# Kernel optimization log

Hardware: AMD Instinct MI355X
Metric: run time of the kernel (lower is better)

## Reference

```python
import jax, jax.numpy as jnp
import numpy as np
from jax import lax

N = 4667      # num vertices (hardcoded in Spatial_Attention_layer)
B = 4         # batch
T = 8         # raw timesteps; (T-2)*3 == 18 after TimeBlock + concat
C_IN = 2      # input features
TP = 18       # concatenated timesteps
HID = 16      # TimeBlock out channels / PCN fc width
N_ROOTS = 500
BRANCH = 2
DEPTH = 3


def _build_tree():
    # Static stand-in for the P/roots/s2rDic dict-based trajectory tree.
    rng = np.random.RandomState(42)
    roots = rng.choice(N, N_ROOTS, replace=False)
    path_node = [int(r) for r in roots]
    levels = []
    prev = list(range(N_ROOTS))
    for _ in range(DEPTH):
        p_idx, c_idx, pn, cn, nxt = [], [], [], [], []
        for pi in prev:
            kids = rng.choice(N, BRANCH, replace=False)
            for c in kids:
                ci = len(path_node)
                path_node.append(int(c))
                p_idx.append(pi); c_idx.append(ci)
                pn.append(path_node[pi]); cn.append(int(c))
                nxt.append(ci)
        levels.append((np.array(p_idx), np.array(c_idx), np.array(pn), np.array(cn)))
        prev = nxt
    leaf_idx = np.array(prev)
    leaf_node = np.array([path_node[i] for i in prev])
    return np.asarray(roots), levels, leaf_idx, leaf_node, len(path_node)

ROOTS, LEVELS, LEAF_IDX, LEAF_NODES, NUM_PATHS = _build_tree()
ROOT_PATH_IDX = np.arange(N_ROOTS)


def setup_inputs() -> dict:
    key = jax.random.key(0)
    ks = jax.random.split(key, 16)
    f = jnp.float32
    rn = lambda k, s: 0.1 * jax.random.normal(k, s, f)
    return {
        "X": jax.random.normal(ks[0], (B, N, T, C_IN), f),
        "X_daily": jax.random.normal(ks[1], (B, N, T, C_IN), f),
        "X_weekly": jax.random.normal(ks[2], (B, N, T, C_IN), f),
        "mask": jnp.zeros((1,), jnp.int32),  # unused in forward (as in source)
        "conv1_w": rn(ks[3], (HID, C_IN, 1, 3)),
        "conv1_b": rn(ks[4], (HID,)),
        "conv2_w": rn(ks[5], (HID, C_IN, 1, 3)),
        "conv2_b": rn(ks[6], (HID,)),
        "W1": rn(ks[7], (HID,)),
        "W2": rn(ks[8], (TP, HID)),
        "W3": rn(ks[9], (TP,)),
        "bs": rn(ks[10], (1, N, N)),
        "Vs": rn(ks[11], (N, N)),
        "fc_w": rn(ks[12], (HID, HID)),
        "fc_b": rn(ks[13], (HID,)),
    }


def reference(X, X_daily, X_weekly, mask, conv1_w, conv1_b, conv2_w, conv2_b,
              W1, W2, W3, bs, Vs, fc_w, fc_b):
    dn = ("NCHW", "OIHW", "NCHW")

    def time_block(Xin):
        # [B,N,T,C] -> [B,C,N,T] -> GLU conv over time -> [B,N,T-2,HID]
        Xp = jnp.transpose(Xin, (0, 3, 1, 2))
        c1 = lax.conv_general_dilated(Xp, conv1_w, (1, 1), "VALID", dimension_numbers=dn) + conv1_b[None, :, None, None]
        c2 = lax.conv_general_dilated(Xp, conv2_w, (1, 1), "VALID", dimension_numbers=dn) + conv2_b[None, :, None, None]
        return jnp.transpose(c1 * jax.nn.sigmoid(c2), (0, 2, 3, 1))

    x = jnp.concatenate([time_block(X), time_block(X_daily), time_block(X_weekly)], axis=2)  # [B,N,18,16]

    # spatial attention
    lhs = jnp.einsum("bnt,tc->bnc", jnp.einsum("bntc,c->bnt", x, W1), W2)   # [B,N,16]
    rhs = jnp.einsum("t,bntc->bnc", W3, x)                                    # [B,N,16]
    product = jnp.einsum("bnc,bmc->bnm", lhs, rhs)                            # [B,N,N]
    S = jnp.einsum("nm,bmk->bnk", Vs, jax.nn.sigmoid(product + bs))           # [B,N,N]
    A = jax.nn.softmax(S, axis=1)

    # PCN tree propagation: h_child = fc(h_parent) * A[:, p, c] + x[c]
    xn = jnp.transpose(x, (1, 0, 2, 3))  # [N,B,18,16]
    H = jnp.zeros((NUM_PATHS, B, TP, HID), x.dtype)
    H = H.at[ROOT_PATH_IDX].set(xn[ROOTS])
    for p_idx, c_idx, pn, cn in LEVELS:
        hp = H[p_idx]                                   # [E,B,18,16]
        a = jnp.transpose(A[:, pn, cn])                 # [E,B]
        hc = (jnp.einsum("ebtc,dc->ebtd", hp, fc_w) + fc_b) * a[:, :, None, None] + xn[cn]
        H = H.at[c_idx].set(hc)

    # mean-pool leaf paths per terminal node; fall back to x for nodes w/o leaves
    leaf_h = H[LEAF_IDX]
    sums = jax.ops.segment_sum(leaf_h, LEAF_NODES, num_segments=N)
    counts = jax.ops.segment_sum(jnp.ones((LEAF_NODES.shape[0],), x.dtype), LEAF_NODES, num_segments=N)
    has_leaf = (counts > 0)[:, None, None, None]
    out_n = jnp.where(has_leaf, sums / jnp.maximum(counts, 1.0)[:, None, None, None], xn)
    return jnp.transpose(out_n, (1, 0, 2, 3))  # [B,N,18,16]
```

## Files before the change

### kernel.cpp

```cpp
#include <hip/hip_runtime.h>
#include <stdint.h>
#include <string.h>

#define NV      4667
#define BB      4
#define TT      8
#define TPX     18
#define HID     16
#define NROOTS  500
#define NPATHS  7500
#define NEDGES  7000
#define NLEAF   4000
#define NP2     4864
#define LDKQ    5120

typedef __bf16 bf16;
typedef bf16  bf16x4 __attribute__((ext_vector_type(4)));
typedef int   i32x4v __attribute__((ext_vector_type(4)));
typedef int   i32x16 __attribute__((ext_vector_type(16)));
typedef const void __attribute__((address_space(1))) gvoid;
typedef void       __attribute__((address_space(3))) svoid;

struct MT19937 {
    uint32_t mt[624]; int pos;
    void seed(uint32_t s) {
        for (int i = 0; i < 624; ++i) { mt[i] = s; s = 1812433253u * (s ^ (s >> 30)) + (uint32_t)i + 1u; }
        pos = 624;
    }
    uint32_t next() {
        if (pos >= 624) {
            for (int i = 0; i < 624; ++i) {
                uint32_t y = (mt[i] & 0x80000000u) | (mt[(i + 1) % 624] & 0x7fffffffu);
                uint32_t v = mt[(i + 397) % 624] ^ (y >> 1);
                if (y & 1u) v ^= 0x9908b0dfu;
                mt[i] = v;
            }
            pos = 0;
        }
        uint32_t y = mt[pos++];
        y ^= y >> 11; y ^= (y << 7) & 0x9d2c5680u; y ^= (y << 15) & 0xefc60000u; y ^= y >> 18;
        return y;
    }
    uint32_t interval(uint32_t mx) {
        if (!mx) return 0;
        uint32_t mask = mx;
        mask |= mask >> 1; mask |= mask >> 2; mask |= mask >> 4; mask |= mask >> 8; mask |= mask >> 16;
        uint32_t v;
        do { v = next() & mask; } while (v > mx);
        return v;
    }
};

struct TreeBlob {
    int path_node[NPATHS];
    int leaf_start[NV + 1];
    int leaf_path[NLEAF];
};

static void build_tree_host(TreeBlob* tb) {
    MT19937 rng; rng.seed(42);
    static int perm[NV];
    auto choice_take = [&](int* out, int k) {
        for (int i = 0; i < NV; ++i) perm[i] = i;
        for (int i = NV - 1; i >= 1; --i) {
            int j = (int)rng.interval((uint32_t)i);
            int t = perm[i]; perm[i] = perm[j]; perm[j] = t;
        }
        for (int i = 0; i < k; ++i) out[i] = perm[i];
    };
    int np_ = 0;
    int roots[NROOTS];
    choice_take(roots, NROOTS);
    for (int i = 0; i < NROOTS; ++i) tb->path_node[np_++] = roots[i];
    int prev_cnt = NROOTS;
    for (int lvl = 0; lvl < 3; ++lvl) {
        int kids[2];
        for (int p = 0; p < prev_cnt; ++p) {
            choice_take(kids, 2);
            tb->path_node[np_++] = kids[0];
            tb->path_node[np_++] = kids[1];
        }
        prev_cnt *= 2;
    }
    static int cnt[NV], cur[NV];
    memset(cnt, 0, sizeof(cnt));
    for (int l = 0; l < NLEAF; ++l) cnt[tb->path_node[3500 + l]]++;
    tb->leaf_start[0] = 0;
    for (int n = 0; n < NV; ++n) tb->leaf_start[n + 1] = tb->leaf_start[n] + cnt[n];
    for (int n = 0; n < NV; ++n) cur[n] = tb->leaf_start[n];
    for (int l = 0; l < NLEAF; ++l) {
        int n = tb->path_node[3500 + l];
        tb->leaf_path[cur[n]++] = 3500 + l;
    }
}

static TreeBlob* get_pinned_tree() {
    static TreeBlob* p = [] {
        TreeBlob* q = nullptr;
        if (hipHostMalloc((void**)&q, sizeof(TreeBlob), 0) != hipSuccess || !q) {
            static TreeBlob fallback;
            q = &fallback;
        }
        build_tree_host(q);
        return q;
    }();
    return p;
}

__global__ void k_timeblock(const float* __restrict__ X, const float* __restrict__ Xd,
                            const float* __restrict__ Xw,
                            const float* __restrict__ w1, const float* __restrict__ b1,
                            const float* __restrict__ w2, const float* __restrict__ b2,
                            float* __restrict__ x) {
    int idx = blockIdx.x * 256 + threadIdx.x;
    if (idx >= BB * NV * 18) return;
    int t = idx % 6;
    int g = (idx / 6) % 3;
    int n = (idx / 18) % NV;
    int b = idx / (18 * NV);
    const float* Xg = (g == 0) ? X : (g == 1) ? Xd : Xw;
    const float* p = Xg + (((size_t)b * NV + n) * TT + t) * 2;
    float v[6];
#pragma unroll
    for (int kk = 0; kk < 3; ++kk) { v[kk * 2 + 0] = p[kk * 2 + 0]; v[kk * 2 + 1] = p[kk * 2 + 1]; }
    float* xo = x + (((size_t)b * NV + n) * TPX + (g * 6 + t)) * HID;
#pragma unroll
    for (int o = 0; o < 16; ++o) {
        float c1 = b1[o], c2 = b2[o];
#pragma unroll
        for (int ci = 0; ci < 2; ++ci)
#pragma unroll
            for (int kk = 0; kk < 3; ++kk) {
                float xv = v[kk * 2 + ci];
                c1 += xv * w1[(o * 2 + ci) * 3 + kk];
                c2 += xv * w2[(o * 2 + ci) * 3 + kk];
            }
        xo[o] = c1 * (1.0f / (1.0f + __expf(-c2)));
    }
}

__global__ void k_lhsrhs(const float* __restrict__ x, const float* __restrict__ W1,
                         const float* __restrict__ W2, const float* __restrict__ W3,
                         float* __restrict__ lhs, float* __restrict__ rhs) {
    int idx = blockIdx.x * 256 + threadIdx.x;
    if (idx >= BB * NV) return;
    const float* xp = x + (size_t)idx * TPX * HID;
    float l[16], r[16];
#pragma unroll
    for (int c = 0; c < 16; ++c) { l[c] = 0.f; r[c] = 0.f; }
    for (int t = 0; t < TPX; ++t) {
        float xt = 0.f, w3 = W3[t];
#pragma unroll
        for (int c = 0; c < 16; ++c) { float xv = xp[t * 16 + c]; xt += xv * W1[c]; r[c] += w3 * xv; }
#pragma unroll
        for (int c = 0; c < 16; ++c) l[c] += xt * W2[t * 16 + c];
    }
    float* lo = lhs + (size_t)idx * 16;
    float* ro = rhs + (size_t)idx * 16;
#pragma unroll
    for (int c = 0; c < 16; ++c) { lo[c] = l[c]; ro[c] = r[c]; }
}

__global__ __launch_bounds__(256)
void k_vsq(const float* __restrict__ Vs, int8_t* __restrict__ Vq,
           float* __restrict__ sA, float* __restrict__ c0) {
    int n = blockIdx.x;
    int t = threadIdx.x;
    int8_t* row_out = Vq + (size_t)n * LDKQ;
    if (n >= NV) {
        for (int m = t * 4; m < LDKQ; m += 1024) *(int*)(row_out + m) = 0;
        if (t == 0) { sA[n] = 0.f; c0[n] = 0.f; }
        return;
    }
    const float* row = Vs + (size_t)n * NV;
    float v[20];
    float mx = 0.f;
#pragma unroll
    for (int i = 0; i < 20; ++i) {
        int m = t + i * 256;
        v[i] = (m < NV) ? row[m] : 0.f;
        mx = fmaxf(mx, fabsf(v[i]));
    }
#pragma unroll
    for (int o = 32; o; o >>= 1) mx = fmaxf(mx, __shfl_xor(mx, o));
    __shared__ float wred[4];
    __shared__ int ired[4];
    if ((t & 63) == 0) wred[t >> 6] = mx;
    __syncthreads();
    mx = fmaxf(fmaxf(wred[0], wred[1]), fmaxf(wred[2], wred[3]));
    mx = fmaxf(mx, 1e-30f);
    float inv = 127.f / mx;
    int qs = 0;
#pragma unroll
    for (int i = 0; i < 20; ++i) {
        int q = (int)rintf(v[i] * inv);
        qs += q;
        row_out[t + i * 256] = (int8_t)q;
    }
#pragma unroll
    for (int o = 32; o; o >>= 1) qs += __shfl_xor(qs, o);
    if ((t & 63) == 0) ired[t >> 6] = qs;
    __syncthreads();
    if (t == 0) {
        int tot = ired[0] + ired[1] + ired[2] + ired[3];
        sA[n] = mx / 32258.f;
        c0[n] = mx * (float)tot / 254.f;
    }
}

__global__ __launch_bounds__(256)
void k_sig(const float* __restrict__ lhs, const float* __restrict__ rhs,
           const float* __restrict__ bs, int8_t* __restrict__ Sq) {
    int m0 = blockIdx.x * 256;
    int k0 = blockIdx.y * 64;
    __shared__ bf16 bss[64 * 260];
    int t = threadIdx.x;

    for (int i = t; i < 256 * 64; i += 256) {
        int row = i >> 6, col = i & 63;
        int mg = m0 + row, kg = k0 + col;
        float v = (mg < NV && kg < NV) ? bs[(size_t)mg * NV + kg] : 0.f;
        bss[col * 260 + row] = (bf16)v;
    }
    __syncthreads();

    int ml = t & 63, kc = t >> 6;
    int mbase = m0 + ml * 4;

    for (int b = 0; b < BB; ++b) {
        float lv[4][16];
#pragma unroll
        for (int r = 0; r < 4; ++r) {
            int mg = mbase + r;
            if (mg < NV) {
                const float4* lp = (const float4*)&lhs[((size_t)b * NV + mg) * 16];
#pragma unroll
                for (int q = 0; q < 4; ++q) {
                    float4 f = lp[q];
                    lv[r][q * 4 + 0] = f.x; lv[r][q * 4 + 1] = f.y;
                    lv[r][q * 4 + 2] = f.z; lv[r][q * 4 + 3] = f.w;
                }
            } else {
#pragma unroll
                for (int c = 0; c < 16; ++c) lv[r][c] = 0.f;
            }
        }
#pragma unroll
        for (int kk = 0; kk < 16; ++kk) {
            int kl = kc * 16 + kk;
            int kg = k0 + kl;
            bool kvalid = (kg < NV);
            float rsv[16];
            if (kvalid) {
                const float4* rp = (const float4*)&rhs[((size_t)b * NV + kg) * 16];
#pragma unroll
                for (int q = 0; q < 4; ++q) {
                    float4 f = rp[q];
                    rsv[q * 4 + 0] = f.x; rsv[q * 4 + 1] = f.y;
                    rsv[q * 4 + 2] = f.z; rsv[q * 4 + 3] = f.w;
                }
            } else {
#pragma unroll
                for (int c = 0; c < 16; ++c) rsv[c] = 0.f;
            }
            bf16x4 bv = *(const bf16x4*)&bss[kl * 260 + ml * 4];
            int pack = 0;
#pragma unroll
            for (int r = 0; r < 4; ++r) {
                float dot = 0.f;
#pragma unroll
                for (int c = 0; c < 16; ++c) dot += lv[r][c] * rsv[c];
                float pv = dot + (float)bv[r];
                float s = 1.0f / (1.0f + __expf(-pv));
                int q = 0;
                if (kvalid && (mbase + r) < NV) q = (int)rintf(254.f * (s - 0.5f));
                pack |= (q & 0xff) << (8 * r);
            }
            *(int*)&Sq[((size_t)b * NP2 + kg) * LDKQ + mbase] = pack;
        }
    }
}

#define STAGE4(dstoff, gptr, kt) { \
    const int8_t* _g = (gptr) + (size_t)(kt) * 128; \
    __builtin_amdgcn_global_load_lds((gvoid*)(_g),                     (svoid*)(sb + (dstoff) + dst0), 16, 0, 0); \
    __builtin_amdgcn_global_load_lds((gvoid*)(_g + (size_t)64 * LDKQ), (svoid*)(sb + (dstoff) + dst0 + 8192), 16, 0, 0); \
    __builtin_amdgcn_global_load_lds((gvoid*)(_g + (size_t)128 * LDKQ),(svoid*)(sb + (dstoff) + dst0 + 16384), 16, 0, 0); \
    __builtin_amdgcn_global_load_lds((gvoid*)(_g + (size_t)192 * LDKQ),(svoid*)(sb + (dstoff) + dst0 + 24576), 16, 0, 0); }

#define READ_G(ar, br, RB, K0) { \
    _Pragma("unroll") for (int mf = 0; mf < 4; ++mf) { \
        ar[mf][0] = *(const i32x4v*)((RB) + abase + mf * 4096 + colks[K0]); \
        ar[mf][1] = *(const i32x4v*)((RB) + abase + mf * 4096 + colks[K0 + 1]); } \
    _Pragma("unroll") for (int nf = 0; nf < 2; ++nf) { \
        br[nf][0] = *(const i32x4v*)((RB) + bbase + nf * 4096 + colks[K0]); \
        br[nf][1] = *(const i32x4v*)((RB) + bbase + nf * 4096 + colks[K0 + 1]); } }

#define MMA_G(ar, br) { \
    __builtin_amdgcn_s_setprio(1); \
    _Pragma("unroll") for (int kk = 0; kk < 2; ++kk) \
    _Pragma("unroll") for (int mf = 0; mf < 4; ++mf) \
    _Pragma("unroll") for (int nf = 0; nf < 2; ++nf) \
        acc[mf][nf] = __builtin_amdgcn_mfma_i32_32x32x32_i8(ar[mf][kk], br[nf][kk], acc[mf][nf], 0, 0, 0); \
    __builtin_amdgcn_s_setprio(0); }

#define WINDOW(RB, SB, TSTAGE) { \
    char* sb = (SB); \
    STAGE4(0, gA, TSTAGE); \
    STAGE4(32768, gB, TSTAGE); \
    READ_G(a0, b0, RB, 0); \
    READ_G(a1, b1, RB, 2); \
    MMA_G(a0, b0); \
    MMA_G(a1, b1); \
    asm volatile("s_waitcnt vmcnt(0)" ::: "memory"); \
    __builtin_amdgcn_s_barrier(); }

__global__ __launch_bounds__(512, 2)
void k_gemm32(const int8_t* __restrict__ Vq, const int8_t* __restrict__ Sq,
              const float* __restrict__ sA, const float* __restrict__ c0,
              float* __restrict__ colsum) {
    extern __shared__ char ldsb[];

    int orig = blockIdx.x;
    int xcd = orig & 7, lin = orig >> 3;
    int wg = (xcd < 4) ? xcd * 181 + lin : 724 + (xcd - 4) * 180 + lin;
    int bi = wg % 19;
    int bk = (wg / 19) % 19;
    int bb = wg / 361;

    int t = threadIdx.x;
    int lane = t & 63, wv = t >> 6;
    int wr = wv >> 2, wc = wv & 3;
    int l31 = lane & 31, hi = lane >> 5;
    int key = (lane & 7) << 4;
    int colks[4];
#pragma unroll
    for (int ks = 0; ks < 4; ++ks) colks[ks] = (ks * 32 + hi * 16) ^ key;
    int abase = wr * 16384 + l31 * 128;
    int bbase = 32768 + wc * 8192 + l31 * 128;

    int rl0 = t >> 3;
    int csw = ((t & 7) << 4) ^ ((rl0 & 7) << 4);
    const int8_t* gA = Vq + ((size_t)(bi * 256) + rl0) * LDKQ + csw;
    const int8_t* gB = Sq + ((size_t)bb * NP2 + (size_t)bk * 256 + rl0) * LDKQ + csw;
    int dst0 = t * 16;

    i32x16 acc[4][2];
#pragma unroll
    for (int i = 0; i < 4; ++i)
#pragma unroll
        for (int j = 0; j < 2; ++j)
#pragma unroll
            for (int r = 0; r < 16; ++r) acc[i][j][r] = 0;

    i32x4v a0[4][2], a1[4][2], b0[2][2], b1[2][2];

    {
        char* sb = ldsb;
        STAGE4(0, gA, 0);
        STAGE4(32768, gB, 0);
    }
    asm volatile("s_waitcnt vmcnt(0)" ::: "memory");
    __builtin_amdgcn_s_barrier();

    for (int i = 0; i < 19; ++i) {
        WINDOW(ldsb,         ldsb + 65536, 2 * i + 1);
        WINDOW(ldsb + 65536, ldsb,         2 * i + 2);
    }

#pragma unroll
    for (int nf = 0; nf < 2; ++nf) {
        int col = bk * 256 + wc * 64 + nf * 32 + l31;
        float csum = 0.f;
#pragma unroll
        for (int mf = 0; mf < 4; ++mf) {
            int rowb = bi * 256 + wr * 128 + mf * 32 + 4 * hi;
#pragma unroll
            for (int g = 0; g < 4; ++g) {
                int rg = rowb + 8 * g;
                float4 sa4 = *(const float4*)&sA[rg];
                float4 c04 = *(const float4*)&c0[rg];
                float sar[4] = {sa4.x, sa4.y, sa4.z, sa4.w};
                float c0r[4] = {c04.x, c04.y, c04.z, c04.w};
#pragma unroll
                for (int r = 0; r < 4; ++r) {
                    float S = sar[r] * (float)acc[mf][nf][g * 4 + r] + c0r[r];
                    csum += ((rg + r) < NV && col < NV) ? __expf(S) : 0.f;
                }
            }
        }
        csum += __shfl_xor(csum, 32);
        if (lane < 32 && col < NV) atomicAdd(&colsum[(size_t)bb * NV + col], csum);
    }
}

__global__ void k_edge(const int8_t* __restrict__ Vq, const int8_t* __restrict__ Sq,
                       const float* __restrict__ sA, const float* __restrict__ c0,
                       const float* __restrict__ colsum, const int* __restrict__ path_node,
                       float* __restrict__ a_edge) {
    int g = blockIdx.x;
    int b = threadIdx.x >> 6;
    int lane = threadIdx.x & 63;
    int e, pbase, cbase;
    if (g < 1000)      { e = g;        pbase = 0;    cbase = 500;  }
    else if (g < 3000) { e = g - 1000; pbase = 500;  cbase = 1500; }
    else               { e = g - 3000; pbase = 1500; cbase = 3500; }
    int pn = path_node[pbase + (e >> 1)];
    int cn = path_node[cbase + e];
    const int8_t* va = Vq + (size_t)pn * LDKQ;
    const int8_t* vb = Sq + ((size_t)b * NP2 + cn) * LDKQ;
    int acc = 0;
    for (int i = lane * 16; i < LDKQ; i += 1024) {
        i32x4v a4 = *(const i32x4v*)(va + i);
        i32x4v b4 = *(const i32x4v*)(vb + i);
#pragma unroll
        for (int w = 0; w < 4; ++w) {
            int aw = a4[w], bw = b4[w];
#pragma unroll
            for (int q = 0; q < 4; ++q)
                acc += (int)(int8_t)(aw >> (8 * q)) * (int)(int8_t)(bw >> (8 * q));
        }
    }
#pragma unroll
    for (int o = 32; o; o >>= 1) acc += __shfl_xor(acc, o);
    if (lane == 0) {
        float S = sA[pn] * (float)acc + c0[pn];
        a_edge[(size_t)g * BB + b] = __expf(S) / colsum[(size_t)b * NV + cn];
    }
}

__global__ void k_root(const float* __restrict__ x, const int* __restrict__ path_node,
                       float* __restrict__ H) {
    int idx = blockIdx.x * 256 + threadIdx.x;
    if (idx >= NROOTS * BB * 288) return;
    int d = idx % 288;
    int b = (idx / 288) % BB;
    int p = idx / (288 * BB);
    int n = path_node[p];
    H[((size_t)p * BB + b) * 288 + d] = x[((size_t)b * NV + n) * 288 + d];
}

__global__ void k_level(const float* __restrict__ x, const int* __restrict__ path_node,
                        const float* __restrict__ fcw, const float* __restrict__ fcb,
                        const float* __restrict__ a_edge, float* __restrict__ H,
                        int E, int pbase, int cbase, int gbase) {
    int idx = blockIdx.x * 256 + threadIdx.x;
    if (idx >= E * BB * 288) return;
    int d = idx & 15;
    int t = (idx >> 4) % TPX;
    int b = (idx / (16 * TPX)) % BB;
    int e = idx / (16 * TPX * BB);
    int pp = pbase + (e >> 1);
    int cp = cbase + e;
    const float* hp = &H[(((size_t)pp * BB + b) * TPX + t) * HID];
    float acc = fcb[d];
#pragma unroll
    for (int c = 0; c < 16; ++c) acc += hp[c] * fcw[d * 16 + c];
    float a = a_edge[(size_t)(gbase + e) * BB + b];
    int cn = path_node[cp];
    float xv = x[(((size_t)b * NV + cn) * TPX + t) * HID + d];
    H[(((size_t)cp * BB + b) * TPX + t) * HID + d] = acc * a + xv;
}

__global__ void k_pool(const float* __restrict__ x, const float* __restrict__ H,
                       const int* __restrict__ leaf_start, const int* __restrict__ leaf_path,
                       float* __restrict__ out) {
    int n = blockIdx.x;
    int s = leaf_start[n], epos = leaf_start[n + 1];
    int cnt = epos - s;
    for (int idx = threadIdx.x; idx < BB * 288; idx += 256) {
        int b = idx / 288, d = idx % 288;
        float v;
        if (cnt == 0) {
            v = x[((size_t)b * NV + n) * 288 + d];
        } else {
            float sum = 0.f;
            for (int l = s; l < epos; ++l) {
                int p = leaf_path[l];
                sum += H[((size_t)p * BB + b) * 288 + d];
            }
            v = sum / (float)cnt;
        }
        out[((size_t)b * NV + n) * 288 + d] = v;
    }
}

extern "C" void kernel_launch(void* const* d_in, const int* in_sizes, int n_in,
                              void* d_out, int out_size, void* d_ws, size_t ws_size,
                              hipStream_t stream) {
    const float* X   = (const float*)d_in[0];
    const float* Xd  = (const float*)d_in[1];
    const float* Xw  = (const float*)d_in[2];
    const float* c1w = (const float*)d_in[4];
    const float* c1b = (const float*)d_in[5];
    const float* c2w = (const float*)d_in[6];
    const float* c2b = (const float*)d_in[7];
    const float* W1  = (const float*)d_in[8];
    const float* W2  = (const float*)d_in[9];
    const float* W3  = (const float*)d_in[10];
    const float* bs  = (const float*)d_in[11];
    const float* Vs  = (const float*)d_in[12];
    const float* fcw = (const float*)d_in[13];
    const float* fcb = (const float*)d_in[14];
    float* out = (float*)d_out;

    TreeBlob* pinned = get_pinned_tree();

    char* w = (char*)d_ws;
    auto alloc = [&](size_t bytes) { char* p = w; w += (bytes + 255) & ~(size_t)255; return p; };
    float*  x      = (float*)alloc((size_t)BB * NV * 288 * 4);
    float*  lhs    = (float*)alloc((size_t)BB * NV * 16 * 4);
    float*  rhs    = (float*)alloc((size_t)BB * NV * 16 * 4);
    float*  colsum = (float*)alloc((size_t)BB * NV * 4);
    float*  aedge  = (float*)alloc((size_t)NEDGES * BB * 4);
    float*  H      = (float*)alloc((size_t)NPATHS * BB * 288 * 4);
    float*  sAr    = (float*)alloc((size_t)NP2 * 4);
    float*  c0r    = (float*)alloc((size_t)NP2 * 4);
    int*    dtree  = (int*)alloc(sizeof(TreeBlob));
    int8_t* Vq     = (int8_t*)alloc((size_t)NP2 * LDKQ);
    int8_t* Sq     = (int8_t*)alloc((size_t)BB * NP2 * LDKQ);

    int* d_path   = dtree;
    int* d_lstart = dtree + NPATHS;
    int* d_lpath  = d_lstart + (NV + 1);

    hipFuncSetAttribute((const void*)k_gemm32, hipFuncAttributeMaxDynamicSharedMemorySize, 131072);

    hipMemcpyAsync(dtree, pinned, sizeof(TreeBlob), hipMemcpyHostToDevice, stream);
    hipMemsetAsync(colsum, 0, (size_t)BB * NV * 4, stream);

    k_timeblock<<<(BB * NV * 18 + 255) / 256, 256, 0, stream>>>(X, Xd, Xw, c1w, c1b, c2w, c2b, x);
    k_lhsrhs<<<(BB * NV + 255) / 256, 256, 0, stream>>>(x, W1, W2, W3, lhs, rhs);
    k_vsq<<<NP2, 256, 0, stream>>>(Vs, Vq, sAr, c0r);
    dim3 sgrid(LDKQ / 256, NP2 / 64);
    k_sig<<<sgrid, 256, 0, stream>>>(lhs, rhs, bs, Sq);
    k_gemm32<<<19 * 19 * BB, 512, 131072, stream>>>(Vq, Sq, sAr, c0r, colsum);
    k_edge<<<NEDGES, 256, 0, stream>>>(Vq, Sq, sAr, c0r, colsum, d_path, aedge);
    k_root<<<(NROOTS * BB * 288 + 255) / 256, 256, 0, stream>>>(x, d_path, H);
    k_level<<<(1000 * BB * 288 + 255) / 256, 256, 0, stream>>>(x, d_path, fcw, fcb, aedge, H, 1000, 0, 500, 0);
    k_level<<<(2000 * BB * 288 + 255) / 256, 256, 0, stream>>>(x, d_path, fcw, fcb, aedge, H, 2000, 500, 1500, 1000);
    k_level<<<(4000 * BB * 288 + 255) / 256, 256, 0, stream>>>(x, d_path, fcw, fcb, aedge, H, 4000, 1500, 3500, 3000);
    k_pool<<<NV, 256, 0, stream>>>(x, H, d_lstart, d_lpath, out);
}
```

Measured before the change: 856.2 us.

## Fuse prep kernels, switch GEMM to 16x16x64 MFMA, vectorize tree levels

```diff
diff --git a/kernel.cpp b/kernel.cpp
--- a/kernel.cpp
+++ b/kernel.cpp
@@ -13,11 +13,12 @@
 #define NLEAF   4000
 #define NP2     4864
 #define LDKQ    5120
+#define NSIGM   20
+#define NSIGK   76
 
 typedef __bf16 bf16;
 typedef bf16  bf16x4 __attribute__((ext_vector_type(4)));
 typedef int   i32x4v __attribute__((ext_vector_type(4)));
-typedef int   i32x16 __attribute__((ext_vector_type(16)));
 typedef const void __attribute__((address_space(1))) gvoid;
 typedef void       __attribute__((address_space(3))) svoid;
 
@@ -162,59 +163,70 @@
 }
 
 __global__ __launch_bounds__(256)
-void k_vsq(const float* __restrict__ Vs, int8_t* __restrict__ Vq,
-           float* __restrict__ sA, float* __restrict__ c0) {
-    int n = blockIdx.x;
-    int t = threadIdx.x;
-    int8_t* row_out = Vq + (size_t)n * LDKQ;
-    if (n >= NV) {
-        for (int m = t * 4; m < LDKQ; m += 1024) *(int*)(row_out + m) = 0;
-        if (t == 0) { sA[n] = 0.f; c0[n] = 0.f; }
-        return;
-    }
-    const float* row = Vs + (size_t)n * NV;
-    float v[20];
-    float mx = 0.f;
-#pragma unroll
-    for (int i = 0; i < 20; ++i) {
-        int m = t + i * 256;
-        v[i] = (m < NV) ? row[m] : 0.f;
-        mx = fmaxf(mx, fabsf(v[i]));
-    }
-#pragma unroll
-    for (int o = 32; o; o >>= 1) mx = fmaxf(mx, __shfl_xor(mx, o));
+void k_prep(const float* __restrict__ Vs, int8_t* __restrict__ Vq,
+            float* __restrict__ sA, float* __restrict__ c0,
+            const float* __restrict__ lhs, const float* __restrict__ rhs,
+            const float* __restrict__ bs, int8_t* __restrict__ Sq,
+            float* __restrict__ colsum) {
     __shared__ float wred[4];
     __shared__ int ired[4];
-    if ((t & 63) == 0) wred[t >> 6] = mx;
-    __syncthreads();
-    mx = fmaxf(fmaxf(wred[0], wred[1]), fmaxf(wred[2], wred[3]));
-    mx = fmaxf(mx, 1e-30f);
-    float inv = 127.f / mx;
-    int qs = 0;
-#pragma unroll
-    for (int i = 0; i < 20; ++i) {
-        int q = (int)rintf(v[i] * inv);
-        qs += q;
-        row_out[t + i * 256] = (int8_t)q;
-    }
-#pragma unroll
-    for (int o = 32; o; o >>= 1) qs += __shfl_xor(qs, o);
-    if ((t & 63) == 0) ired[t >> 6] = qs;
-    __syncthreads();
-    if (t == 0) {
-        int tot = ired[0] + ired[1] + ired[2] + ired[3];
-        sA[n] = mx / 32258.f;
-        c0[n] = mx * (float)tot / 254.f;
-    }
-}
-
-__global__ __launch_bounds__(256)
-void k_sig(const float* __restrict__ lhs, const float* __restrict__ rhs,
-           const float* __restrict__ bs, int8_t* __restrict__ Sq) {
-    int m0 = blockIdx.x * 256;
-    int k0 = blockIdx.y * 64;
     __shared__ bf16 bss[64 * 260];
+    int blk = blockIdx.x;
     int t = threadIdx.x;
+
+    if (blk < NP2) {
+        if (blk < 19) {
+#pragma unroll
+            for (int u = 0; u < 4; ++u) {
+                int ii = blk * 1024 + u * 256 + t;
+                if (ii < BB * NV) colsum[ii] = 0.f;
+            }
+        }
+        int n = blk;
+        int8_t* row_out = Vq + (size_t)n * LDKQ;
+        if (n >= NV) {
+            for (int m = t * 4; m < LDKQ; m += 1024) *(int*)(row_out + m) = 0;
+            if (t == 0) { sA[n] = 0.f; c0[n] = 0.f; }
+            return;
+        }
+        const float* row = Vs + (size_t)n * NV;
+        float v[20];
+        float mx = 0.f;
+#pragma unroll
+        for (int i = 0; i < 20; ++i) {
+            int m = t + i * 256;
+            v[i] = (m < NV) ? row[m] : 0.f;
+            mx = fmaxf(mx, fabsf(v[i]));
+        }
+#pragma unroll
+        for (int o = 32; o; o >>= 1) mx = fmaxf(mx, __shfl_xor(mx, o));
+        if ((t & 63) == 0) wred[t >> 6] = mx;
+        __syncthreads();
+        mx = fmaxf(fmaxf(wred[0], wred[1]), fmaxf(wred[2], wred[3]));
+        mx = fmaxf(mx, 1e-30f);
+        float inv = 127.f / mx;
+        int qs = 0;
+#pragma unroll
+        for (int i = 0; i < 20; ++i) {
+            int q = (int)rintf(v[i] * inv);
+            qs += q;
+            row_out[t + i * 256] = (int8_t)q;
+        }
+#pragma unroll
+        for (int o = 32; o; o >>= 1) qs += __shfl_xor(qs, o);
+        if ((t & 63) == 0) ired[t >> 6] = qs;
+        __syncthreads();
+        if (t == 0) {
+            int tot = ired[0] + ired[1] + ired[2] + ired[3];
+            sA[n] = mx / 32258.f;
+            c0[n] = mx * (float)tot / 254.f;
+        }
+        return;
+    }
+
+    int bid = blk - NP2;
+    int m0 = (bid % NSIGM) * 256;
+    int k0 = (bid / NSIGM) * 64;
 
     for (int i = t; i < 256 * 64; i += 256) {
         int row = i >> 6, col = i & 63;
@@ -281,42 +293,35 @@
     }
 }
 
-#define STAGE4(dstoff, gptr, kt) { \
-    const int8_t* _g = (gptr) + (size_t)(kt) * 128; \
-    __builtin_amdgcn_global_load_lds((gvoid*)(_g),                     (svoid*)(sb + (dstoff) + dst0), 16, 0, 0); \
-    __builtin_amdgcn_global_load_lds((gvoid*)(_g + (size_t)64 * LDKQ), (svoid*)(sb + (dstoff) + dst0 + 8192), 16, 0, 0); \
-    __builtin_amdgcn_global_load_lds((gvoid*)(_g + (size_t)128 * LDKQ),(svoid*)(sb + (dstoff) + dst0 + 16384), 16, 0, 0); \
-    __builtin_amdgcn_global_load_lds((gvoid*)(_g + (size_t)192 * LDKQ),(svoid*)(sb + (dstoff) + dst0 + 24576), 16, 0, 0); }
-
-#define READ_G(ar, br, RB, K0) { \
-    _Pragma("unroll") for (int mf = 0; mf < 4; ++mf) { \
-        ar[mf][0] = *(const i32x4v*)((RB) + abase + mf * 4096 + colks[K0]); \
-        ar[mf][1] = *(const i32x4v*)((RB) + abase + mf * 4096 + colks[K0 + 1]); } \
-    _Pragma("unroll") for (int nf = 0; nf < 2; ++nf) { \
-        br[nf][0] = *(const i32x4v*)((RB) + bbase + nf * 4096 + colks[K0]); \
-        br[nf][1] = *(const i32x4v*)((RB) + bbase + nf * 4096 + colks[K0 + 1]); } }
-
-#define MMA_G(ar, br) { \
+#define BUF1 65536
+
+#define STAGE8(BUF, kt) { \
+    const int8_t* _ga = gA + (size_t)(kt) * 128; \
+    const int8_t* _gb = gB + (size_t)(kt) * 128; \
+    __builtin_amdgcn_global_load_lds((gvoid*)(_ga),                      (svoid*)(ldsb + (BUF) + dst0), 16, 0, 0); \
+    __builtin_amdgcn_global_load_lds((gvoid*)(_ga + (size_t)64  * LDKQ), (svoid*)(ldsb + (BUF) + dst0 + 8192), 16, 0, 0); \
+    __builtin_amdgcn_global_load_lds((gvoid*)(_ga + (size_t)128 * LDKQ), (svoid*)(ldsb + (BUF) + dst0 + 16384), 16, 0, 0); \
+    __builtin_amdgcn_global_load_lds((gvoid*)(_ga + (size_t)192 * LDKQ), (svoid*)(ldsb + (BUF) + dst0 + 24576), 16, 0, 0); \
+    __builtin_amdgcn_global_load_lds((gvoid*)(_gb),                      (svoid*)(ldsb + (BUF) + 32768 + dst0), 16, 0, 0); \
+    __builtin_amdgcn_global_load_lds((gvoid*)(_gb + (size_t)64  * LDKQ), (svoid*)(ldsb + (BUF) + 32768 + dst0 + 8192), 16, 0, 0); \
+    __builtin_amdgcn_global_load_lds((gvoid*)(_gb + (size_t)128 * LDKQ), (svoid*)(ldsb + (BUF) + 32768 + dst0 + 16384), 16, 0, 0); \
+    __builtin_amdgcn_global_load_lds((gvoid*)(_gb + (size_t)192 * LDKQ), (svoid*)(ldsb + (BUF) + 32768 + dst0 + 24576), 16, 0, 0); }
+
+#define RD(BUF, KS) { \
+    _Pragma("unroll") for (int mf = 0; mf < 8; ++mf) \
+        af[mf] = *(const i32x4v*)(ldsb + (BUF) + arow + mf * 2048 + ck[KS]); \
+    _Pragma("unroll") for (int nj = 0; nj < 4; ++nj) \
+        bf[nj] = *(const i32x4v*)(ldsb + (BUF) + brow + nj * 2048 + ck[KS]); }
+
+#define MM() { \
     __builtin_amdgcn_s_setprio(1); \
-    _Pragma("unroll") for (int kk = 0; kk < 2; ++kk) \
-    _Pragma("unroll") for (int mf = 0; mf < 4; ++mf) \
-    _Pragma("unroll") for (int nf = 0; nf < 2; ++nf) \
-        acc[mf][nf] = __builtin_amdgcn_mfma_i32_32x32x32_i8(ar[mf][kk], br[nf][kk], acc[mf][nf], 0, 0, 0); \
+    _Pragma("unroll") for (int mf = 0; mf < 8; ++mf) \
+    _Pragma("unroll") for (int nj = 0; nj < 4; ++nj) \
+        acc[mf][nj] = __builtin_amdgcn_mfma_i32_16x16x64_i8(af[mf], bf[nj], acc[mf][nj], 0, 0, 0); \
     __builtin_amdgcn_s_setprio(0); }
 
-#define WINDOW(RB, SB, TSTAGE) { \
-    char* sb = (SB); \
-    STAGE4(0, gA, TSTAGE); \
-    STAGE4(32768, gB, TSTAGE); \
-    READ_G(a0, b0, RB, 0); \
-    READ_G(a1, b1, RB, 2); \
-    MMA_G(a0, b0); \
-    MMA_G(a1, b1); \
-    asm volatile("s_waitcnt vmcnt(0)" ::: "memory"); \
-    __builtin_amdgcn_s_barrier(); }
-
 __global__ __launch_bounds__(512, 2)
-void k_gemm32(const int8_t* __restrict__ Vq, const int8_t* __restrict__ Sq,
+void k_gemm16(const int8_t* __restrict__ Vq, const int8_t* __restrict__ Sq,
               const float* __restrict__ sA, const float* __restrict__ c0,
               float* __restrict__ colsum) {
     extern __shared__ char ldsb[];
@@ -331,13 +336,14 @@
     int t = threadIdx.x;
     int lane = t & 63, wv = t >> 6;
     int wr = wv >> 2, wc = wv & 3;
-    int l31 = lane & 31, hi = lane >> 5;
-    int key = (lane & 7) << 4;
-    int colks[4];
-#pragma unroll
-    for (int ks = 0; ks < 4; ++ks) colks[ks] = (ks * 32 + hi * 16) ^ key;
-    int abase = wr * 16384 + l31 * 128;
-    int bbase = 32768 + wc * 8192 + l31 * 128;
+    int lr = lane & 15, lg = lane >> 4;
+    int key = (lr & 7) << 4;
+
+    int ck[2];
+    ck[0] = (lg * 16) ^ key;
+    ck[1] = (64 + lg * 16) ^ key;
+    int arow = wr * 16384 + lr * 128;
+    int brow = 32768 + wc * 8192 + lr * 128;
 
     int rl0 = t >> 3;
     int csw = ((t & 7) << 4) ^ ((rl0 & 7) << 4);
@@ -345,52 +351,50 @@
     const int8_t* gB = Sq + ((size_t)bb * NP2 + (size_t)bk * 256 + rl0) * LDKQ + csw;
     int dst0 = t * 16;
 
-    i32x16 acc[4][2];
-#pragma unroll
-    for (int i = 0; i < 4; ++i)
-#pragma unroll
-        for (int j = 0; j < 2; ++j)
-#pragma unroll
-            for (int r = 0; r < 16; ++r) acc[i][j][r] = 0;
-
-    i32x4v a0[4][2], a1[4][2], b0[2][2], b1[2][2];
-
-    {
-        char* sb = ldsb;
-        STAGE4(0, gA, 0);
-        STAGE4(32768, gB, 0);
-    }
+    i32x4v acc[8][4];
+#pragma unroll
+    for (int i = 0; i < 8; ++i)
+#pragma unroll
+        for (int j = 0; j < 4; ++j) acc[i][j] = i32x4v{0, 0, 0, 0};
+
+    i32x4v af[8], bf[4];
+
+    STAGE8(0, 0);
     asm volatile("s_waitcnt vmcnt(0)" ::: "memory");
     __builtin_amdgcn_s_barrier();
 
-    for (int i = 0; i < 19; ++i) {
-        WINDOW(ldsb,         ldsb + 65536, 2 * i + 1);
-        WINDOW(ldsb + 65536, ldsb,         2 * i + 2);
-    }
-
-#pragma unroll
-    for (int nf = 0; nf < 2; ++nf) {
-        int col = bk * 256 + wc * 64 + nf * 32 + l31;
+    for (int ti = 0; ti < 38; ++ti) {
+        int cur = (ti & 1) ? BUF1 : 0;
+        int nxt = cur ^ BUF1;
+        STAGE8(nxt, ti + 1);
+        RD(cur, 0);
+        MM();
+        RD(cur, 1);
+        MM();
+        asm volatile("s_waitcnt vmcnt(0)" ::: "memory");
+        __builtin_amdgcn_s_barrier();
+    }
+
+#pragma unroll
+    for (int nj = 0; nj < 4; ++nj) {
+        int col = bk * 256 + wc * 64 + nj * 16 + lr;
         float csum = 0.f;
 #pragma unroll
-        for (int mf = 0; mf < 4; ++mf) {
-            int rowb = bi * 256 + wr * 128 + mf * 32 + 4 * hi;
-#pragma unroll
-            for (int g = 0; g < 4; ++g) {
-                int rg = rowb + 8 * g;
-                float4 sa4 = *(const float4*)&sA[rg];
-                float4 c04 = *(const float4*)&c0[rg];
-                float sar[4] = {sa4.x, sa4.y, sa4.z, sa4.w};
-                float c0r[4] = {c04.x, c04.y, c04.z, c04.w};
-#pragma unroll
-                for (int r = 0; r < 4; ++r) {
-                    float S = sar[r] * (float)acc[mf][nf][g * 4 + r] + c0r[r];
-                    csum += ((rg + r) < NV && col < NV) ? __expf(S) : 0.f;
-                }
-            }
-        }
+        for (int mf = 0; mf < 8; ++mf) {
+            int rowb = bi * 256 + wr * 128 + mf * 16 + lg * 4;
+            float4 sa4 = *(const float4*)&sA[rowb];
+            float4 c04 = *(const float4*)&c0[rowb];
+            float sar[4] = {sa4.x, sa4.y, sa4.z, sa4.w};
+            float c0r[4] = {c04.x, c04.y, c04.z, c04.w};
+#pragma unroll
+            for (int r = 0; r < 4; ++r) {
+                float S = sar[r] * (float)acc[mf][nj][r] + c0r[r];
+                csum += ((rowb + r) < NV && col < NV) ? __expf(S) : 0.f;
+            }
+        }
+        csum += __shfl_xor(csum, 16);
         csum += __shfl_xor(csum, 32);
-        if (lane < 32 && col < NV) atomicAdd(&colsum[(size_t)bb * NV + col], csum);
+        if (lane < 16 && col < NV) atomicAdd(&colsum[(size_t)bb * NV + col], csum);
     }
 }
 
@@ -429,37 +433,51 @@
     }
 }
 
-__global__ void k_root(const float* __restrict__ x, const int* __restrict__ path_node,
-                       float* __restrict__ H) {
+__global__ __launch_bounds__(256)
+void k_level(const float* __restrict__ x, const int* __restrict__ path_node,
+             const float* __restrict__ fcw, const float* __restrict__ fcb,
+             const float* __restrict__ a_edge, float* __restrict__ H,
+             int E, int pbase, int cbase, int gbase, int lvl1) {
     int idx = blockIdx.x * 256 + threadIdx.x;
-    if (idx >= NROOTS * BB * 288) return;
-    int d = idx % 288;
-    int b = (idx / 288) % BB;
-    int p = idx / (288 * BB);
-    int n = path_node[p];
-    H[((size_t)p * BB + b) * 288 + d] = x[((size_t)b * NV + n) * 288 + d];
-}
-
-__global__ void k_level(const float* __restrict__ x, const int* __restrict__ path_node,
-                        const float* __restrict__ fcw, const float* __restrict__ fcb,
-                        const float* __restrict__ a_edge, float* __restrict__ H,
-                        int E, int pbase, int cbase, int gbase) {
-    int idx = blockIdx.x * 256 + threadIdx.x;
-    if (idx >= E * BB * 288) return;
-    int d = idx & 15;
-    int t = (idx >> 4) % TPX;
-    int b = (idx / (16 * TPX)) % BB;
-    int e = idx / (16 * TPX * BB);
+    if (idx >= E * BB * TPX) return;
+    int t = idx % TPX;
+    int b = (idx / TPX) & 3;
+    int e = idx / (TPX * BB);
     int pp = pbase + (e >> 1);
+    const float* hp;
+    if (lvl1) {
+        int pn = path_node[pp];
+        hp = &x[(((size_t)b * NV + pn) * TPX + t) * HID];
+    } else {
+        hp = &H[(((size_t)pp * BB + b) * TPX + t) * HID];
+    }
+    float h[16];
+    const float4* hp4 = (const float4*)hp;
+#pragma unroll
+    for (int q = 0; q < 4; ++q) {
+        float4 f = hp4[q];
+        h[q * 4 + 0] = f.x; h[q * 4 + 1] = f.y; h[q * 4 + 2] = f.z; h[q * 4 + 3] = f.w;
+    }
+    float a = a_edge[(size_t)(gbase + e) * BB + b];
     int cp = cbase + e;
-    const float* hp = &H[(((size_t)pp * BB + b) * TPX + t) * HID];
-    float acc = fcb[d];
-#pragma unroll
-    for (int c = 0; c < 16; ++c) acc += hp[c] * fcw[d * 16 + c];
-    float a = a_edge[(size_t)(gbase + e) * BB + b];
     int cn = path_node[cp];
-    float xv = x[(((size_t)b * NV + cn) * TPX + t) * HID + d];
-    H[(((size_t)cp * BB + b) * TPX + t) * HID + d] = acc * a + xv;
+    const float4* xv4 = (const float4*)&x[(((size_t)b * NV + cn) * TPX + t) * HID];
+    float4* outp = (float4*)&H[(((size_t)cp * BB + b) * TPX + t) * HID];
+#pragma unroll
+    for (int q = 0; q < 4; ++q) {
+        float4 xv = xv4[q];
+        float o[4];
+#pragma unroll
+        for (int j = 0; j < 4; ++j) {
+            int d = q * 4 + j;
+            float acc = fcb[d];
+#pragma unroll
+            for (int c = 0; c < 16; ++c) acc += h[c] * fcw[d * 16 + c];
+            o[j] = acc * a;
+        }
+        float4 ov; ov.x = o[0] + xv.x; ov.y = o[1] + xv.y; ov.z = o[2] + xv.z; ov.w = o[3] + xv.w;
+        outp[q] = ov;
+    }
 }
 
 __global__ void k_pool(const float* __restrict__ x, const float* __restrict__ H,
@@ -524,21 +542,17 @@
     int* d_lstart = dtree + NPATHS;
     int* d_lpath  = d_lstart + (NV + 1);
 
-    hipFuncSetAttribute((const void*)k_gemm32, hipFuncAttributeMaxDynamicSharedMemorySize, 131072);
+    hipFuncSetAttribute((const void*)k_gemm16, hipFuncAttributeMaxDynamicSharedMemorySize, 131072);
 
     hipMemcpyAsync(dtree, pinned, sizeof(TreeBlob), hipMemcpyHostToDevice, stream);
-    hipMemsetAsync(colsum, 0, (size_t)BB * NV * 4, stream);
 
     k_timeblock<<<(BB * NV * 18 + 255) / 256, 256, 0, stream>>>(X, Xd, Xw, c1w, c1b, c2w, c2b, x);
     k_lhsrhs<<<(BB * NV + 255) / 256, 256, 0, stream>>>(x, W1, W2, W3, lhs, rhs);
-    k_vsq<<<NP2, 256, 0, stream>>>(Vs, Vq, sAr, c0r);
-    dim3 sgrid(LDKQ / 256, NP2 / 64);
-    k_sig<<<sgrid, 256, 0, stream>>>(lhs, rhs, bs, Sq);
-    k_gemm32<<<19 * 19 * BB, 512, 131072, stream>>>(Vq, Sq, sAr, c0r, colsum);
+    k_prep<<<NP2 + NSIGM * NSIGK, 256, 0, stream>>>(Vs, Vq, sAr, c0r, lhs, rhs, bs, Sq, colsum);
+    k_gemm16<<<19 * 19 * BB, 512, 131072, stream>>>(Vq, Sq, sAr, c0r, colsum);
     k_edge<<<NEDGES, 256, 0, stream>>>(Vq, Sq, sAr, c0r, colsum, d_path, aedge);
-    k_root<<<(NROOTS * BB * 288 + 255) / 256, 256, 0, stream>>>(x, d_path, H);
-    k_level<<<(1000 * BB * 288 + 255) / 256, 256, 0, stream>>>(x, d_path, fcw, fcb, aedge, H, 1000, 0, 500, 0);
-    k_level<<<(2000 * BB * 288 + 255) / 256, 256, 0, stream>>>(x, d_path, fcw, fcb, aedge, H, 2000, 500, 1500, 1000);
-    k_level<<<(4000 * BB * 288 + 255) / 256, 256, 0, stream>>>(x, d_path, fcw, fcb, aedge, H, 4000, 1500, 3500, 3000);
+    k_level<<<(1000 * BB * TPX + 255) / 256, 256, 0, stream>>>(x, d_path, fcw, fcb, aedge, H, 1000, 0, 500, 0, 1);
+    k_level<<<(2000 * BB * TPX + 255) / 256, 256, 0, stream>>>(x, d_path, fcw, fcb, aedge, H, 2000, 500, 1500, 1000, 0);
+    k_level<<<(4000 * BB * TPX + 255) / 256, 256, 0, stream>>>(x, d_path, fcw, fcb, aedge, H, 4000, 1500, 3500, 3000, 0);
     k_pool<<<NV, 256, 0, stream>>>(x, H, d_lstart, d_lpath, out);
 }
```

Result: faster. 725.8 us (-15.2%).
